# Performance work log

Hardware: AMD Instinct MI355X
Metric: run time of the kernel (lower is better)

## Reference

```python
import jax, jax.numpy as jnp
import numpy as np

D_IN = 1024
D_OUT = 1024
B = 4
S = 2048


def setup_inputs() -> dict:
    key = jax.random.key(0)
    kx, kq, kk, kv = jax.random.split(key, 4)
    x = jax.random.normal(kx, (B, S, D_IN), dtype=jnp.float32)
    # Linear weights stored as [d_in, d_out] so projection is x @ W
    sc = 1.0 / np.sqrt(D_IN)
    Wq = jax.random.normal(kq, (D_IN, D_OUT), dtype=jnp.float32) * sc
    Wk = jax.random.normal(kk, (D_IN, D_OUT), dtype=jnp.float32) * sc
    Wv = jax.random.normal(kv, (D_IN, D_OUT), dtype=jnp.float32) * sc
    return {"x": x, "Wq": Wq, "Wk": Wk, "Wv": Wv}


def reference(x, Wq, Wk, Wv):
    # q, k, v: [b, s, d_out]
    q = jnp.einsum("bsd,de->bse", x, Wq)
    k = jnp.einsum("bsd,de->bse", x, Wk)
    v = jnp.einsum("bsd,de->bse", x, Wv)
    s = q.shape[1]
    # raw scores [b, s, s]
    scores = jnp.einsum("bqd,bkd->bqk", q, k)
    # causal mask: disallow key j > query i (see notes re: original mask bug)
    causal = jnp.triu(jnp.ones((s, s), dtype=bool), k=1)
    scores = jnp.where(causal[None, :, :], -jnp.inf, scores)
    scale = 1.0 / jnp.sqrt(jnp.asarray(k.shape[-1], dtype=scores.dtype))
    att_weights = jax.nn.softmax(scores * scale, axis=-1)
    # dropout p=0.0 -> identity
    att_output = jnp.einsum("bqk,bkd->bqd", att_weights, v)
    return att_output, att_weights
```

## Files before the change

kernel.cpp:

```cpp
#include <hip/hip_runtime.h>
#include <stdint.h>

#define DIM 1024
#define SEQ 2048
#define NB 4

typedef unsigned short u16;
typedef __bf16 bf16x8 __attribute__((ext_vector_type(8)));
typedef float floatx4 __attribute__((ext_vector_type(4)));

__device__ __forceinline__ u16 f32_to_bf16(float f) {
  union { float f; unsigned u; } v; v.f = f;
  unsigned r = v.u + 0x7FFFu + ((v.u >> 16) & 1u);
  return (u16)(r >> 16);
}

__device__ __forceinline__ void async16(const void* g, void* l) {
  __builtin_amdgcn_global_load_lds(
      (__attribute__((address_space(1))) unsigned int*)g,
      (__attribute__((address_space(3))) unsigned int*)l, 16, 0, 0);
}

__global__ __launch_bounds__(256) void k_prep(const float* __restrict__ x,
                                              const float* __restrict__ Wq,
                                              const float* __restrict__ Wk,
                                              const float* __restrict__ Wv,
                                              u16* __restrict__ xb,
                                              u16* __restrict__ wt) {
  __shared__ u16 tile[32][33];
  const int bid = blockIdx.x;
  const int tid = threadIdx.x;
  if (bid < 4096) {
    int i = bid * 256 + tid;
    float4 a = ((const float4*)x)[i * 2];
    float4 b = ((const float4*)x)[i * 2 + 1];
    ushort4 o0, o1;
    o0.x = f32_to_bf16(a.x); o0.y = f32_to_bf16(a.y);
    o0.z = f32_to_bf16(a.z); o0.w = f32_to_bf16(a.w);
    o1.x = f32_to_bf16(b.x); o1.y = f32_to_bf16(b.y);
    o1.z = f32_to_bf16(b.z); o1.w = f32_to_bf16(b.w);
    ((ushort4*)xb)[i * 2] = o0;
    ((ushort4*)xb)[i * 2 + 1] = o1;
  } else {
    int t = bid - 4096;
    int z = t >> 10;
    int ti = t & 1023;
    int c0 = (ti & 31) * 32, r0 = (ti >> 5) * 32;
    const float* src = (z == 0) ? Wq : (z == 1) ? Wk : Wv;
    u16* d = wt + (size_t)z * DIM * DIM;
    int tx = tid & 31, ty = tid >> 5;
    #pragma unroll
    for (int dy = 0; dy < 32; dy += 8)
      tile[ty + dy][tx] = f32_to_bf16(src[(size_t)(r0 + ty + dy) * DIM + c0 + tx]);
    __syncthreads();
    #pragma unroll
    for (int dy = 0; dy < 32; dy += 8)
      d[(size_t)(c0 + ty + dy) * DIM + r0 + tx] = tile[tx][ty + dy];
  }
}


#define STG(PG, STBASE, SLOT, H, I, KT)                                        \
  async16((PG) + (size_t)((H) * 128 + (I) * 64) * DIM + (KT) * 64,             \
          (STBASE) + (SLOT) * 16384 + (H) * 8192 + (I) * 4096)

#define PHASE(SLOT, KS, MH, RDB, STGS, SYNC)                                   \
  {                                                                            \
    const int go_ = (KS) ? ga1 : ga0;                                          \
    const u16* pa_ = aRd + (SLOT) * 16384;                                     \
    if (RDB) {                                                                 \
      const u16* pb_ = bRd + (SLOT) * 16384;                                   \
      _Pragma("unroll") for (int n = 0; n < 4; ++n)                            \
          bfr[n] = *(const bf16x8*)(pb_ + n * 1024 + go_);                     \
    }                                                                          \
    _Pragma("unroll") for (int m = 0; m < 4; ++m)                              \
        af[m] = *(const bf16x8*)(pa_ + ((MH) * 4 + m) * 1024 + go_);           \
    STGS                                                                       \
    __builtin_amdgcn_s_barrier();                                              \
    asm volatile("s_waitcnt lgkmcnt(0)");                                      \
    __builtin_amdgcn_s_setprio(1);                                             \
    _Pragma("unroll") for (int m = 0; m < 4; ++m)                              \
        _Pragma("unroll") for (int n = 0; n < 4; ++n)                          \
            acc[(MH) * 4 + m][n] = __builtin_amdgcn_mfma_f32_16x16x32_bf16(    \
                af[m], bfr[n], acc[(MH) * 4 + m][n], 0, 0, 0);                 \
    __builtin_amdgcn_s_setprio(0);                                             \
    SYNC                                                                       \
    __builtin_amdgcn_s_barrier();                                              \
  }

__global__ __launch_bounds__(512) void k_proj8(const u16* __restrict__ xb,
                                               const u16* __restrict__ wt,
                                               u16* __restrict__ qk,
                                               u16* __restrict__ vT) {
  __shared__ u16 lds[65536];
  const int wg = ((blockIdx.x & 7) * 48) + (blockIdx.x >> 3);
  const int tid = threadIdx.x;
  const int lane = tid & 63;
  const int wid = tid >> 6;

  const u16 *A, *Bt;
  u16* Cout;
  int ldc;
  if (wg < 256) {
    const int z = wg >> 7;
    const int r = wg & 127;
    const int mt = r >> 2, nt = r & 3;
    A = xb + (size_t)mt * 256 * DIM;
    Bt = wt + (size_t)z * DIM * DIM + (size_t)nt * 256 * DIM;
    Cout = qk + (size_t)z * (NB * SEQ * DIM) + (size_t)mt * 256 * DIM + nt * 256;
    ldc = DIM;
  } else {
    const int r = wg - 256;
    const int mt = r & 3, nt = r >> 2;
    A = wt + (size_t)2 * DIM * DIM + (size_t)mt * 256 * DIM;
    Bt = xb + (size_t)nt * 256 * DIM;
    Cout = vT + (size_t)(nt >> 3) * (DIM * SEQ) + (size_t)mt * 256 * SEQ
              + (nt & 7) * 256;
    ldc = SEQ;
  }

  const int srow = wid * 8 + (lane >> 3);
  const int gsrc = (lane & 7) ^ ((lane >> 3) & 7);
  const u16* pga = A + (size_t)srow * DIM + gsrc * 8;
  const u16* pgb = Bt + (size_t)srow * DIM + gsrc * 8;
  u16* stA = lds + wid * 512;
  u16* stB = lds + 32768 + wid * 512;

  const int wr = wid >> 2, wc = wid & 3;
  const int lrow = lane & 15, quad = lane >> 4;
  const int s = lrow & 7;
  const u16* aRd = lds + (wr * 128 + lrow) * 64;
  const u16* bRd = lds + 32768 + (wc * 64 + lrow) * 64;
  const int ga0 = (quad ^ s) << 3;
  const int ga1 = ga0 ^ 32;

  floatx4 acc[8][4] = {};
  bf16x8 af[4], bfr[4];

  STG(pga, stA, 0, 0, 0, 0); STG(pga, stA, 0, 0, 1, 0);
  STG(pga, stA, 0, 1, 0, 0); STG(pga, stA, 0, 1, 1, 0);
  STG(pgb, stB, 0, 0, 0, 0); STG(pgb, stB, 0, 0, 1, 0);
  STG(pgb, stB, 0, 1, 0, 0); STG(pgb, stB, 0, 1, 1, 0);
  STG(pgb, stB, 1, 0, 0, 1); STG(pgb, stB, 1, 0, 1, 1);
  asm volatile("s_waitcnt vmcnt(2)");
  __builtin_amdgcn_sched_barrier(0);
  __builtin_amdgcn_s_barrier();

  const int NITER = DIM / 128;
  for (int t = 0; t < NITER; ++t) {
    const bool more = (t + 1 < NITER);
    const int kA1 = 2 * t + 1;
    const int kN = 2 * t + 2;
    const int kB1n = 2 * t + 3;

    PHASE(0, 0, 0, 1,
          { STG(pga, stA, 1, 0, 0, kA1); STG(pga, stA, 1, 0, 1, kA1); }, {})
    PHASE(0, 0, 1, 0,
          { STG(pga, stA, 1, 1, 0, kA1); STG(pga, stA, 1, 1, 1, kA1); }, {})
    PHASE(0, 1, 0, 1,
          { STG(pgb, stB, 1, 1, 0, kA1); STG(pgb, stB, 1, 1, 1, kA1); }, {})
    PHASE(0, 1, 1, 0,
          { if (more) { STG(pgb, stB, 0, 0, 0, kN); STG(pgb, stB, 0, 0, 1, kN); } },
          { if (more) { asm volatile("s_waitcnt vmcnt(2)"); }
            else      { asm volatile("s_waitcnt vmcnt(0)"); }
            __builtin_amdgcn_sched_barrier(0); })
    PHASE(1, 0, 0, 1,
          { if (more) { STG(pgb, stB, 0, 1, 0, kN); STG(pgb, stB, 0, 1, 1, kN); } }, {})
    PHASE(1, 0, 1, 0,
          { if (more) { STG(pga, stA, 0, 0, 0, kN); STG(pga, stA, 0, 0, 1, kN); } }, {})
    PHASE(1, 1, 0, 1,
          { if (more) { STG(pga, stA, 0, 1, 0, kN); STG(pga, stA, 0, 1, 1, kN); } }, {})
    PHASE(1, 1, 1, 0,
          { if (more) { STG(pgb, stB, 1, 0, 0, kB1n); STG(pgb, stB, 1, 0, 1, kB1n); } },
          { if (more) { asm volatile("s_waitcnt vmcnt(2)");
                        __builtin_amdgcn_sched_barrier(0); } })
  }

  asm volatile("s_waitcnt vmcnt(0)");

  u16* C = Cout + (size_t)(wr * 128 + quad * 4) * ldc + wc * 64 + lrow;
  #pragma unroll
  for (int m = 0; m < 8; ++m)
    #pragma unroll
    for (int rr = 0; rr < 4; ++rr)
      #pragma unroll
      for (int n = 0; n < 4; ++n)
        C[(size_t)(m * 16 + rr) * ldc + n * 16] = f32_to_bf16(acc[m][n][rr]);
}

__device__ __forceinline__ void mfma_core128(const u16* __restrict__ A, int lda,
                                             const u16* __restrict__ Bt, int ldb,
                                             int kchunks, u16* lds,
                                             floatx4 acc[4][4]) {
  const int tid = threadIdx.x;
  const int lane = tid & 63;
  const int wid = tid >> 6;
  u16* lds_a = lds;
  u16* lds_b = lds + 16384;

  const int srow4 = lane >> 4;
  const int sgr = lane & 15;
  const int gbase = sgr ^ srow4;
  const u16* ag0 = A + (size_t)(wid * 32 + srow4) * lda + gbase * 8;
  const u16* ag1 = A + (size_t)(wid * 32 + srow4) * lda + (gbase ^ 4) * 8;
  const u16* bg0 = Bt + (size_t)(wid * 32 + srow4) * ldb + gbase * 8;
  const u16* bg1 = Bt + (size_t)(wid * 32 + srow4) * ldb + (gbase ^ 4) * 8;
  u16* la = lds_a + wid * 4096;
  u16* lb = lds_b + wid * 4096;

  const int wm = (wid >> 1) * 64, wn = (wid & 1) * 64;
  const int lrow = lane & 15, quad = lane >> 4;
  const int s = lrow & 7;
  const u16* pa = lds_a + (wm + lrow) * 128;
  const u16* pb = lds_b + (wn + lrow) * 128;

  for (int kt = 0; kt < kchunks; ++kt) {
    #pragma unroll
    for (int c = 0; c < 8; ++c) {
      const u16* sa = ((c & 1) ? ag1 : ag0) + (size_t)(c * 4) * lda;
      async16(sa, la + c * 512);
    }
    #pragma unroll
    for (int c = 0; c < 8; ++c) {
      const u16* sb = ((c & 1) ? bg1 : bg0) + (size_t)(c * 4) * ldb;
      async16(sb, lb + c * 512);
    }
    ag0 += 128; ag1 += 128; bg0 += 128; bg1 += 128;
    __syncthreads();
    #pragma unroll
    for (int ks = 0; ks < 4; ++ks) {
      const int g = (((ks << 2) | quad) ^ s) << 3;
      bf16x8 af[4], bfr[4];
      #pragma unroll
      for (int t = 0; t < 4; ++t) af[t] = *(const bf16x8*)(pa + t * 2048 + g);
      #pragma unroll
      for (int t = 0; t < 4; ++t) bfr[t] = *(const bf16x8*)(pb + t * 2048 + g);
      #pragma unroll
      for (int i = 0; i < 4; ++i)
        #pragma unroll
        for (int j = 0; j < 4; ++j)
          acc[i][j] = __builtin_amdgcn_mfma_f32_16x16x32_bf16(af[i], bfr[j],
                                                              acc[i][j], 0, 0, 0);
    }
    __syncthreads();
  }
}

__global__ __launch_bounds__(256) void k_scores(const u16* __restrict__ q,
                                                const u16* __restrict__ k,
                                                float* __restrict__ w) {
  const int id = blockIdx.x;
  const int b = id & 3;
  int t = id >> 2;
  int mt = (int)((sqrtf(8.0f * (float)t + 1.0f) - 1.0f) * 0.5f);
  while ((mt + 1) * (mt + 2) / 2 <= t) ++mt;
  while (mt * (mt + 1) / 2 > t) --mt;
  const int nt = t - mt * (mt + 1) / 2;
  __shared__ u16 lds[32768];
  floatx4 acc[4][4] = {};
  mfma_core128(q + (size_t)b * SEQ * DIM + (size_t)mt * 128 * DIM, DIM,
               k + (size_t)b * SEQ * DIM + (size_t)nt * 128 * DIM, DIM,
               DIM / 128, lds, acc);
  const int lane = threadIdx.x & 63, wid = threadIdx.x >> 6;
  const int wm = (wid >> 1) * 64, wn = (wid & 1) * 64;
  const int lrow = lane & 15, quad = lane >> 4;
  float* C = w + (size_t)b * SEQ * SEQ
               + (size_t)(mt * 128 + wm + quad * 4) * SEQ + nt * 128 + wn + lrow;
  #pragma unroll
  for (int i = 0; i < 4; ++i)
    #pragma unroll
    for (int rr = 0; rr < 4; ++rr)
      #pragma unroll
      for (int j = 0; j < 4; ++j)
        C[(size_t)(i * 16 + rr) * SEQ + j * 16] = acc[i][j][rr] * 0.03125f;
}

__global__ __launch_bounds__(256) void k_softmax(float* __restrict__ w,
                                                 u16* __restrict__ P) {
  const int r = blockIdx.x;
  const int i = r & (SEQ - 1);
  const int len = i + 1;
  const int plen4 = (((i >> 7) + 1) << 7) >> 2;
  float4* srow = (float4*)(w + (size_t)r * SEQ);
  ushort4* prow = (ushort4*)(P + (size_t)r * SEQ);
  const int tid = threadIdx.x;
  const int lane = tid & 63, wid = tid >> 6;
  __shared__ float rm[4], rs[4];

  float4 e[2];
  float mx = -1e30f;
  #pragma unroll
  for (int u = 0; u < 2; ++u) {
    int q4 = tid + u * 256;
    int j0 = q4 * 4;
    float4 v = make_float4(-1e30f, -1e30f, -1e30f, -1e30f);
    if (j0 < len) {
      v = srow[q4];
      v.x = (j0 + 0 < len) ? v.x : -1e30f;
      v.y = (j0 + 1 < len) ? v.y : -1e30f;
      v.z = (j0 + 2 < len) ? v.z : -1e30f;
      v.w = (j0 + 3 < len) ? v.w : -1e30f;
    }
    e[u] = v;
    mx = fmaxf(mx, fmaxf(fmaxf(v.x, v.y), fmaxf(v.z, v.w)));
  }
  #pragma unroll
  for (int o = 32; o >= 1; o >>= 1) mx = fmaxf(mx, __shfl_xor(mx, o, 64));
  if (lane == 0) rm[wid] = mx;
  __syncthreads();
  mx = fmaxf(fmaxf(rm[0], rm[1]), fmaxf(rm[2], rm[3]));

  float sum = 0.f;
  #pragma unroll
  for (int u = 0; u < 2; ++u) {
    e[u].x = __expf(e[u].x - mx);
    e[u].y = __expf(e[u].y - mx);
    e[u].z = __expf(e[u].z - mx);
    e[u].w = __expf(e[u].w - mx);
    sum += e[u].x + e[u].y + e[u].z + e[u].w;
  }
  #pragma unroll
  for (int o = 32; o >= 1; o >>= 1) sum += __shfl_xor(sum, o, 64);
  if (lane == 0) rs[wid] = sum;
  __syncthreads();
  sum = rs[0] + rs[1] + rs[2] + rs[3];
  const float inv = 1.0f / sum;

  #pragma unroll
  for (int u = 0; u < 2; ++u) {
    int q4 = tid + u * 256;
    int j0 = q4 * 4;
    float4 v;
    v.x = (j0 + 0 < len) ? e[u].x * inv : 0.f;
    v.y = (j0 + 1 < len) ? e[u].y * inv : 0.f;
    v.z = (j0 + 2 < len) ? e[u].z * inv : 0.f;
    v.w = (j0 + 3 < len) ? e[u].w * inv : 0.f;
    srow[q4] = v;
    if (q4 < plen4) {
      ushort4 p;
      p.x = f32_to_bf16(v.x); p.y = f32_to_bf16(v.y);
      p.z = f32_to_bf16(v.z); p.w = f32_to_bf16(v.w);
      prow[q4] = p;
    }
  }
}

__global__ __launch_bounds__(256) void k_pv(const u16* __restrict__ P,
                                            const u16* __restrict__ vT,
                                            float* __restrict__ out) {
  const int id = blockIdx.x;
  const int mt = 15 - (id >> 5);
  const int nt = (id >> 2) & 7;
  const int b = id & 3;
  __shared__ u16 lds[32768];
  floatx4 acc[4][4] = {};
  mfma_core128(P + (size_t)b * SEQ * SEQ + (size_t)mt * 128 * SEQ, SEQ,
               vT + (size_t)b * DIM * SEQ + (size_t)nt * 128 * SEQ, SEQ,
               mt + 1, lds, acc);
  const int lane = threadIdx.x & 63, wid = threadIdx.x >> 6;
  const int wm = (wid >> 1) * 64, wn = (wid & 1) * 64;
  const int lrow = lane & 15, quad = lane >> 4;
  float* C = out + (size_t)b * SEQ * DIM
                 + (size_t)(mt * 128 + wm + quad * 4) * DIM + nt * 128 + wn + lrow;
  #pragma unroll
  for (int i = 0; i < 4; ++i)
    #pragma unroll
    for (int rr = 0; rr < 4; ++rr)
      #pragma unroll
      for (int j = 0; j < 4; ++j)
        C[(size_t)(i * 16 + rr) * DIM + j * 16] = acc[i][j][rr];
}

extern "C" void kernel_launch(void* const* d_in, const int* in_sizes, int n_in,
                              void* d_out, int out_size, void* d_ws, size_t ws_size,
                              hipStream_t stream) {
  const float* x  = (const float*)d_in[0];
  const float* Wq = (const float*)d_in[1];
  const float* Wk = (const float*)d_in[2];
  const float* Wv = (const float*)d_in[3];
  float* att_out = (float*)d_out;
  float* att_w   = (float*)d_out + 8388608;

  u16* xb = (u16*)d_ws;
  u16* wt = xb + 8388608;
  u16* qk = wt + 3145728;
  u16* vT = qk + 16777216;
  u16* P  = vT + 8388608;

  k_prep<<<7168, 256, 0, stream>>>(x, Wq, Wk, Wv, xb, wt);
  k_proj8<<<384, 512, 0, stream>>>(xb, wt, qk, vT);
  k_scores<<<544, 256, 0, stream>>>(qk, qk + 8388608, att_w);
  k_softmax<<<8192, 256, 0, stream>>>(att_w, P);
  k_pv<<<512, 256, 0, stream>>>(P, vT, att_out);
}
```

Measured before the change: 268.4 us.

## Reuse pipelined 256x256 GEMM core for causal score kernel

Pulls the software-pipelined 256x256 MFMA main loop out of the projection kernel into a shared device function. The causal score kernel now uses it with 512-thread blocks on 256x256 lower-triangular tiles, replacing the 128x128 tiles and their simple synchronized loop. The aim is more data reuse per LDS load and better overlap of global loads with MFMA work. In exchange the grid drops to 144 blocks, fewer than the CU count, and diagonal tiles compute more masked-out work.

```diff
diff --git a/kernel.cpp b/kernel.cpp
--- a/kernel.cpp
+++ b/kernel.cpp
@@ -88,53 +88,12 @@
     __builtin_amdgcn_s_barrier();                                              \
   }
 
-__global__ __launch_bounds__(512) void k_proj8(const u16* __restrict__ xb,
-                                               const u16* __restrict__ wt,
-                                               u16* __restrict__ qk,
-                                               u16* __restrict__ vT) {
-  __shared__ u16 lds[65536];
-  const int wg = ((blockIdx.x & 7) * 48) + (blockIdx.x >> 3);
-  const int tid = threadIdx.x;
-  const int lane = tid & 63;
-  const int wid = tid >> 6;
-
-  const u16 *A, *Bt;
-  u16* Cout;
-  int ldc;
-  if (wg < 256) {
-    const int z = wg >> 7;
-    const int r = wg & 127;
-    const int mt = r >> 2, nt = r & 3;
-    A = xb + (size_t)mt * 256 * DIM;
-    Bt = wt + (size_t)z * DIM * DIM + (size_t)nt * 256 * DIM;
-    Cout = qk + (size_t)z * (NB * SEQ * DIM) + (size_t)mt * 256 * DIM + nt * 256;
-    ldc = DIM;
-  } else {
-    const int r = wg - 256;
-    const int mt = r & 3, nt = r >> 2;
-    A = wt + (size_t)2 * DIM * DIM + (size_t)mt * 256 * DIM;
-    Bt = xb + (size_t)nt * 256 * DIM;
-    Cout = vT + (size_t)(nt >> 3) * (DIM * SEQ) + (size_t)mt * 256 * SEQ
-              + (nt & 7) * 256;
-    ldc = SEQ;
-  }
-
-  const int srow = wid * 8 + (lane >> 3);
-  const int gsrc = (lane & 7) ^ ((lane >> 3) & 7);
-  const u16* pga = A + (size_t)srow * DIM + gsrc * 8;
-  const u16* pgb = Bt + (size_t)srow * DIM + gsrc * 8;
-  u16* stA = lds + wid * 512;
-  u16* stB = lds + 32768 + wid * 512;
-
-  const int wr = wid >> 2, wc = wid & 3;
-  const int lrow = lane & 15, quad = lane >> 4;
-  const int s = lrow & 7;
-  const u16* aRd = lds + (wr * 128 + lrow) * 64;
-  const u16* bRd = lds + 32768 + (wc * 64 + lrow) * 64;
-  const int ga0 = (quad ^ s) << 3;
-  const int ga1 = ga0 ^ 32;
-
-  floatx4 acc[8][4] = {};
+__device__ __forceinline__ void core256(const u16* __restrict__ pga,
+                                        const u16* __restrict__ pgb,
+                                        const u16* aRd, const u16* bRd,
+                                        u16* stA, u16* stB,
+                                        int ga0, int ga1,
+                                        floatx4 acc[8][4], int NITER) {
   bf16x8 af[4], bfr[4];
 
   STG(pga, stA, 0, 0, 0, 0); STG(pga, stA, 0, 0, 1, 0);
@@ -146,7 +105,6 @@
   __builtin_amdgcn_sched_barrier(0);
   __builtin_amdgcn_s_barrier();
 
-  const int NITER = DIM / 128;
   for (int t = 0; t < NITER; ++t) {
     const bool more = (t + 1 < NITER);
     const int kA1 = 2 * t + 1;
@@ -177,6 +135,56 @@
   }
 
   asm volatile("s_waitcnt vmcnt(0)");
+}
+
+__global__ __launch_bounds__(512) void k_proj8(const u16* __restrict__ xb,
+                                               const u16* __restrict__ wt,
+                                               u16* __restrict__ qk,
+                                               u16* __restrict__ vT) {
+  __shared__ u16 lds[65536];
+  const int wg = ((blockIdx.x & 7) * 48) + (blockIdx.x >> 3);
+  const int tid = threadIdx.x;
+  const int lane = tid & 63;
+  const int wid = tid >> 6;
+
+  const u16 *A, *Bt;
+  u16* Cout;
+  int ldc;
+  if (wg < 256) {
+    const int z = wg >> 7;
+    const int r = wg & 127;
+    const int mt = r >> 2, nt = r & 3;
+    A = xb + (size_t)mt * 256 * DIM;
+    Bt = wt + (size_t)z * DIM * DIM + (size_t)nt * 256 * DIM;
+    Cout = qk + (size_t)z * (NB * SEQ * DIM) + (size_t)mt * 256 * DIM + nt * 256;
+    ldc = DIM;
+  } else {
+    const int r = wg - 256;
+    const int mt = r & 3, nt = r >> 2;
+    A = wt + (size_t)2 * DIM * DIM + (size_t)mt * 256 * DIM;
+    Bt = xb + (size_t)nt * 256 * DIM;
+    Cout = vT + (size_t)(nt >> 3) * (DIM * SEQ) + (size_t)mt * 256 * SEQ
+              + (nt & 7) * 256;
+    ldc = SEQ;
+  }
+
+  const int srow = wid * 8 + (lane >> 3);
+  const int gsrc = (lane & 7) ^ ((lane >> 3) & 7);
+  const u16* pga = A + (size_t)srow * DIM + gsrc * 8;
+  const u16* pgb = Bt + (size_t)srow * DIM + gsrc * 8;
+  u16* stA = lds + wid * 512;
+  u16* stB = lds + 32768 + wid * 512;
+
+  const int wr = wid >> 2, wc = wid & 3;
+  const int lrow = lane & 15, quad = lane >> 4;
+  const int s = lrow & 7;
+  const u16* aRd = lds + (wr * 128 + lrow) * 64;
+  const u16* bRd = lds + 32768 + (wc * 64 + lrow) * 64;
+  const int ga0 = (quad ^ s) << 3;
+  const int ga1 = ga0 ^ 32;
+
+  floatx4 acc[8][4] = {};
+  core256(pga, pgb, aRd, bRd, stA, stB, ga0, ga1, acc, DIM / 128);
 
   u16* C = Cout + (size_t)(wr * 128 + quad * 4) * ldc + wc * 64 + lrow;
   #pragma unroll
@@ -186,6 +194,54 @@
       #pragma unroll
       for (int n = 0; n < 4; ++n)
         C[(size_t)(m * 16 + rr) * ldc + n * 16] = f32_to_bf16(acc[m][n][rr]);
+}
+
+__global__ __launch_bounds__(512) void k_scores(const u16* __restrict__ q,
+                                                const u16* __restrict__ k,
+                                                float* __restrict__ w) {
+  __shared__ u16 lds[65536];
+  const int wg = ((blockIdx.x & 7) * 18) + (blockIdx.x >> 3);
+  const int b = wg / 36;
+  const int t = wg % 36;
+  int mt = (int)((sqrtf(8.0f * (float)t + 1.0f) - 1.0f) * 0.5f);
+  while ((mt + 1) * (mt + 2) / 2 <= t) ++mt;
+  while (mt * (mt + 1) / 2 > t) --mt;
+  const int nt = t - mt * (mt + 1) / 2;
+
+  const u16* A  = q + (size_t)b * SEQ * DIM + (size_t)mt * 256 * DIM;
+  const u16* Bt = k + (size_t)b * SEQ * DIM + (size_t)nt * 256 * DIM;
+
+  const int tid = threadIdx.x;
+  const int lane = tid & 63;
+  const int wid = tid >> 6;
+  const int srow = wid * 8 + (lane >> 3);
+  const int gsrc = (lane & 7) ^ ((lane >> 3) & 7);
+  const u16* pga = A + (size_t)srow * DIM + gsrc * 8;
+  const u16* pgb = Bt + (size_t)srow * DIM + gsrc * 8;
+  u16* stA = lds + wid * 512;
+  u16* stB = lds + 32768 + wid * 512;
+
+  const int wr = wid >> 2, wc = wid & 3;
+  const int lrow = lane & 15, quad = lane >> 4;
+  const int s = lrow & 7;
+  const u16* aRd = lds + (wr * 128 + lrow) * 64;
+  const u16* bRd = lds + 32768 + (wc * 64 + lrow) * 64;
+  const int ga0 = (quad ^ s) << 3;
+  const int ga1 = ga0 ^ 32;
+
+  floatx4 acc[8][4] = {};
+  core256(pga, pgb, aRd, bRd, stA, stB, ga0, ga1, acc, DIM / 128);
+
+  float* C = w + (size_t)b * SEQ * SEQ
+               + (size_t)(mt * 256 + wr * 128 + quad * 4) * SEQ
+               + nt * 256 + wc * 64 + lrow;
+  #pragma unroll
+  for (int m = 0; m < 8; ++m)
+    #pragma unroll
+    for (int rr = 0; rr < 4; ++rr)
+      #pragma unroll
+      for (int n = 0; n < 4; ++n)
+        C[(size_t)(m * 16 + rr) * SEQ + n * 16] = acc[m][n][rr] * 0.03125f;
 }
 
 __device__ __forceinline__ void mfma_core128(const u16* __restrict__ A, int lda,
@@ -244,35 +300,6 @@
     }
     __syncthreads();
   }
-}
-
-__global__ __launch_bounds__(256) void k_scores(const u16* __restrict__ q,
-                                                const u16* __restrict__ k,
-                                                float* __restrict__ w) {
-  const int id = blockIdx.x;
-  const int b = id & 3;
-  int t = id >> 2;
-  int mt = (int)((sqrtf(8.0f * (float)t + 1.0f) - 1.0f) * 0.5f);
-  while ((mt + 1) * (mt + 2) / 2 <= t) ++mt;
-  while (mt * (mt + 1) / 2 > t) --mt;
-  const int nt = t - mt * (mt + 1) / 2;
-  __shared__ u16 lds[32768];
-  floatx4 acc[4][4] = {};
-  mfma_core128(q + (size_t)b * SEQ * DIM + (size_t)mt * 128 * DIM, DIM,
-               k + (size_t)b * SEQ * DIM + (size_t)nt * 128 * DIM, DIM,
-               DIM / 128, lds, acc);
-  const int lane = threadIdx.x & 63, wid = threadIdx.x >> 6;
-  const int wm = (wid >> 1) * 64, wn = (wid & 1) * 64;
-  const int lrow = lane & 15, quad = lane >> 4;
-  float* C = w + (size_t)b * SEQ * SEQ
-               + (size_t)(mt * 128 + wm + quad * 4) * SEQ + nt * 128 + wn + lrow;
-  #pragma unroll
-  for (int i = 0; i < 4; ++i)
-    #pragma unroll
-    for (int rr = 0; rr < 4; ++rr)
-      #pragma unroll
-      for (int j = 0; j < 4; ++j)
-        C[(size_t)(i * 16 + rr) * SEQ + j * 16] = acc[i][j][rr] * 0.03125f;
 }
 
 __global__ __launch_bounds__(256) void k_softmax(float* __restrict__ w,
@@ -389,7 +416,7 @@
 
   k_prep<<<7168, 256, 0, stream>>>(x, Wq, Wk, Wv, xb, wt);
   k_proj8<<<384, 512, 0, stream>>>(xb, wt, qk, vT);
-  k_scores<<<544, 256, 0, stream>>>(qk, qk + 8388608, att_w);
+  k_scores<<<144, 512, 0, stream>>>(qk, qk + 8388608, att_w);
   k_softmax<<<8192, 256, 0, stream>>>(att_w, P);
   k_pv<<<512, 256, 0, stream>>>(P, vT, att_out);
 }
```

Measured after the change: 265.5 us. About the same (-1.1%).
